# Kernel tuning notes

Measured on AMD Instinct MI355X. Metric: run time of the kernel, lower is better.

Reference implementation:

```python
import jax, jax.numpy as jnp
import numpy as np

B, USER_DIM, ITEM_DIM, LATENT = 8192, 3706, 6040, 512


def setup_inputs() -> dict:
    key = jax.random.key(0)
    kx, kwu, kwi = jax.random.split(key, 3)
    scale_u = 1.0 / np.sqrt(USER_DIM)
    scale_i = 1.0 / np.sqrt(ITEM_DIM)
    return {
        "x": jax.random.normal(kx, (B, USER_DIM + ITEM_DIM), dtype=jnp.float32),
        "Wu": jax.random.normal(kwu, (LATENT, USER_DIM), dtype=jnp.float32) * scale_u,
        "bu": jnp.zeros((LATENT,), dtype=jnp.float32),
        "Wi": jax.random.normal(kwi, (LATENT, ITEM_DIM), dtype=jnp.float32) * scale_i,
        "bi": jnp.zeros((LATENT,), dtype=jnp.float32),
    }


def reference(x, Wu, bu, Wi, bi):
    # mDA encode: linear + relu for each tower
    user_emb = jax.nn.relu(x[:, :USER_DIM] @ Wu.T + bu)   # [B, LATENT]
    item_emb = jax.nn.relu(x[:, -ITEM_DIM:] @ Wi.T + bi)  # [B, LATENT]
    # torch.mm(u, i.T).diag() == row-wise dot product (same math, O(B*d) not O(B^2*d))
    diag = jnp.einsum("bd,bd->b", user_emb, item_emb)     # [B]
    return diag[:, None]                                   # [B, 1]
```

## Files before the change

kernel.cpp:

```cpp
#include <hip/hip_runtime.h>
#include <hip/hip_bf16.h>
#include <stdint.h>

#define USER_DIM 3706
#define ITEM_DIM 6040
#define LATENT   512
#define BATCH    8192
#define XCOLS    (USER_DIM + ITEM_DIM)
#define KPAD_U   3712
#define KPAD_I   6144

typedef float f32x4 __attribute__((ext_vector_type(4)));
typedef short bf16x8 __attribute__((ext_vector_type(8)));

#define VMCNT(n) asm volatile("s_waitcnt vmcnt(" #n ")" ::: "memory")
#define LGKM0    asm volatile("s_waitcnt lgkmcnt(0)" ::: "memory")

static __device__ __forceinline__ unsigned short f2bf(float f) {
    union { float f; unsigned int u; } v; v.f = f;
    unsigned int u = v.u;
    u += 0x7fffu + ((u >> 16) & 1u);
    return (unsigned short)(u >> 16);
}
static __device__ __forceinline__ float bf2f(unsigned int b) {
    union { unsigned int u; float f; } v; v.u = b << 16; return v.f;
}
static __device__ __forceinline__ void gload16(const void* g, void* l) {
    __builtin_amdgcn_global_load_lds(
        (const __attribute__((address_space(1))) void*)g,
        (__attribute__((address_space(3))) void*)l, 16, 0, 0);
}
static __device__ __forceinline__ void BARRIER() {
    __builtin_amdgcn_sched_barrier(0);
    __builtin_amdgcn_s_barrier();
    __builtin_amdgcn_sched_barrier(0);
}

__global__ void convert_w(const float* __restrict__ W, unsigned short* __restrict__ Wb,
                          int K, int Kpad) {
    int c = blockIdx.x * blockDim.x + threadIdx.x;
    int r = blockIdx.y;
    if (c >= Kpad) return;
    unsigned short o = 0;
    if (c < K) o = f2bf(W[(size_t)r * K + c]);
    Wb[(size_t)r * Kpad + c] = o;
}

__global__ __launch_bounds__(256, 3) void gemm_fused(
    const float* __restrict__ X,
    const unsigned short* __restrict__ WuB, const float* __restrict__ bu,
    const unsigned short* __restrict__ WiB,
    unsigned short* __restrict__ Uemb,
    unsigned short* __restrict__ P0, unsigned short* __restrict__ P1)
{
    __shared__ unsigned short sA2[2][64 * 64];
    __shared__ unsigned short sB2[2][64 * 64];

    const int tid  = threadIdx.x;
    const int lane = tid & 63;
    const int wid  = tid >> 6;
    const int wm   = wid >> 1;
    const int wn   = wid & 1;

    const int bid = blockIdx.x;
    const int swz = (bid & 7) * 96 + (bid >> 3);
    const int g4  = swz >> 2;
    const int nb  = swz & 3;

    int mb, k0, nt, xoff, Kpad;
    const unsigned short* WB;
    bool isUser; int kh = 0;
    if (g4 % 3 == 0) {
        isUser = true;  mb = g4 / 3;
        k0 = 0; nt = KPAD_U / 32; xoff = 0; Kpad = KPAD_U; WB = WuB;
    } else {
        const int q = g4 - (g4 / 3 + 1);
        isUser = false; mb = q >> 1; kh = q & 1;
        k0 = kh * 96; nt = 96; xoff = USER_DIM; Kpad = KPAD_I; WB = WiB;
    }

    const int l8  = lane >> 3;
    const int c8w = lane & 7;
    const int s8  = c8w ^ l8;
    const int spr = s8 >> 2;
    const int skc = (s8 & 3) * 8;

    float4 raf[2][2];

    auto ALOAD = [&](int t) {
        const int kb = t * 32;
        #pragma unroll
        for (int o = 0; o < 2; ++o) {
            const int sego = wid * 16 + o * 8 + l8;
            const int grow = mb * 128 + sego * 2 + spr;
            const int xc   = xoff + kb + skc;
            const float* s = X + (size_t)grow * XCOLS + xc;
            if (xc + 8 > XCOLS) s = X;
            raf[o][0] = *(const float4*)s;
            raf[o][1] = *(const float4*)(s + 4);
        }
    };
    auto AWRITE = [&](int buf) {
        unsigned short* sA = sA2[buf];
        #pragma unroll
        for (int o = 0; o < 2; ++o) {
            const int sego = wid * 16 + o * 8 + l8;
            uint4 w;
            w.x = (unsigned)f2bf(raf[o][0].x) | ((unsigned)f2bf(raf[o][0].y) << 16);
            w.y = (unsigned)f2bf(raf[o][0].z) | ((unsigned)f2bf(raf[o][0].w) << 16);
            w.z = (unsigned)f2bf(raf[o][1].x) | ((unsigned)f2bf(raf[o][1].y) << 16);
            w.w = (unsigned)f2bf(raf[o][1].z) | ((unsigned)f2bf(raf[o][1].w) << 16);
            *(uint4*)(sA + sego * 64 + c8w * 8) = w;
        }
    };
    auto ISSUE_B = [&](int t, int buf) {
        const int kb = t * 32;
        unsigned short* sB = sB2[buf];
        #pragma unroll
        for (int j = 0; j < 2; ++j) {
            const int i  = wid * 2 + j;
            const int rt = (i * 8 + l8) * 2 + spr;
            const unsigned short* s =
                WB + (size_t)(nb * 128 + rt) * Kpad + kb + skc;
            gload16(s, sB + i * 512);
        }
    };

    const int fr   = lane & 15;
    const int g    = lane >> 4;
    const int rc8  = ((((fr & 1) * 4) + g) ^ (fr >> 1)) * 8;
    const int aro  = (wm * 32 + (fr >> 1)) * 64 + rc8;
    const int bro  = (wn * 32 + (fr >> 1)) * 64 + rc8;

    f32x4 acc[4][4];
    #pragma unroll
    for (int i = 0; i < 4; ++i)
        #pragma unroll
        for (int j = 0; j < 4; ++j) acc[i][j] = (f32x4)0.0f;

    auto COMPUTE = [&](int buf) {
        const unsigned short* sA = sA2[buf];
        const unsigned short* sB = sB2[buf];
        bf16x8 af[4], bfr[4];
        #pragma unroll
        for (int mi = 0; mi < 4; ++mi)
            af[mi] = *(const bf16x8*)(sA + aro + mi * 512);
        #pragma unroll
        for (int ni = 0; ni < 4; ++ni)
            bfr[ni] = *(const bf16x8*)(sB + bro + ni * 512);
        __builtin_amdgcn_s_setprio(1);
        #pragma unroll
        for (int mi = 0; mi < 4; ++mi)
            #pragma unroll
            for (int ni = 0; ni < 4; ++ni)
                acc[mi][ni] = __builtin_amdgcn_mfma_f32_16x16x32_bf16(
                    af[mi], bfr[ni], acc[mi][ni], 0, 0, 0);
        __builtin_amdgcn_s_setprio(0);
    };

    ALOAD(k0);
    ISSUE_B(k0, 0);
    AWRITE(0);
    ALOAD(k0 + 1);
    LGKM0;
    VMCNT(4);
    BARRIER();
    ISSUE_B(k0 + 1, 1);

    #pragma unroll 2
    for (int t = 0; t < nt - 2; ++t) {
        const int cur = t & 1;
        COMPUTE(cur);
        AWRITE(cur ^ 1);
        ALOAD(k0 + t + 2);
        LGKM0;
        BARRIER();
        ISSUE_B(k0 + t + 2, cur);
        VMCNT(6);
        BARRIER();
    }
    COMPUTE(0);
    AWRITE(1);
    LGKM0;
    BARRIER();
    VMCNT(0);
    BARRIER();
    COMPUTE(1);

    const int cb = nb * 128 + wn * 64;
    const int rb = mb * 128 + wm * 64 + (lane >> 4) * 4;
    if (isUser) {
        #pragma unroll
        for (int ni = 0; ni < 4; ++ni) {
            const int col = cb + ni * 16 + fr;
            const float bv = bu[col];
            #pragma unroll
            for (int mi = 0; mi < 4; ++mi) {
                f32x4 v = acc[mi][ni];
                #pragma unroll
                for (int r = 0; r < 4; ++r) {
                    const int row = rb + mi * 16 + r;
                    Uemb[(size_t)row * LATENT + col] = f2bf(fmaxf(v[r] + bv, 0.0f));
                }
            }
        }
    } else {
        unsigned short* P = kh ? P1 : P0;
        #pragma unroll
        for (int ni = 0; ni < 4; ++ni) {
            const int col = cb + ni * 16 + fr;
            #pragma unroll
            for (int mi = 0; mi < 4; ++mi) {
                f32x4 v = acc[mi][ni];
                #pragma unroll
                for (int r = 0; r < 4; ++r) {
                    const int row = rb + mi * 16 + r;
                    P[(size_t)row * LATENT + col] = f2bf(v[r]);
                }
            }
        }
    }
}

__global__ void rowdot(const unsigned short* __restrict__ U,
                       const unsigned short* __restrict__ P0,
                       const unsigned short* __restrict__ P1,
                       const float* __restrict__ bi,
                       float* __restrict__ out) {
    const int lane = threadIdx.x & 63;
    const int w    = threadIdx.x >> 6;
    const int row  = blockIdx.x * 4 + w;
    const size_t base = (size_t)row * LATENT + lane * 8;
    const uint4 uv = *(const uint4*)(U  + base);
    const uint4 p0 = *(const uint4*)(P0 + base);
    const uint4 p1 = *(const uint4*)(P1 + base);
    const float4 b0 = *(const float4*)(bi + lane * 8);
    const float4 b1 = *(const float4*)(bi + lane * 8 + 4);
    const float bb[8] = {b0.x, b0.y, b0.z, b0.w, b1.x, b1.y, b1.z, b1.w};
    const unsigned int* up = (const unsigned int*)&uv;
    const unsigned int* q0 = (const unsigned int*)&p0;
    const unsigned int* q1 = (const unsigned int*)&p1;
    float acc = 0.0f;
    #pragma unroll
    for (int q = 0; q < 4; ++q) {
        float ilo = fmaxf(bf2f(q0[q] & 0xffffu) + bf2f(q1[q] & 0xffffu) + bb[2 * q], 0.0f);
        float ihi = fmaxf(bf2f(q0[q] >> 16)     + bf2f(q1[q] >> 16)     + bb[2 * q + 1], 0.0f);
        acc += bf2f(up[q] & 0xffffu) * ilo;
        acc += bf2f(up[q] >> 16)     * ihi;
    }
    #pragma unroll
    for (int off = 32; off >= 1; off >>= 1)
        acc += __shfl_xor(acc, off, 64);
    if (lane == 0) out[row] = acc;
}

extern "C" void kernel_launch(void* const* d_in, const int* in_sizes, int n_in,
                              void* d_out, int out_size, void* d_ws, size_t ws_size,
                              hipStream_t stream) {
    const float* x  = (const float*)d_in[0];
    const float* Wu = (const float*)d_in[1];
    const float* bu = (const float*)d_in[2];
    const float* Wi = (const float*)d_in[3];
    const float* bi = (const float*)d_in[4];
    float* out = (float*)d_out;

    unsigned short* WuB  = (unsigned short*)d_ws;
    unsigned short* WiB  = WuB + (size_t)LATENT * KPAD_U;
    unsigned short* Uemb = WiB + (size_t)LATENT * KPAD_I;
    unsigned short* P0   = Uemb + (size_t)BATCH * LATENT;
    unsigned short* P1   = P0   + (size_t)BATCH * LATENT;

    convert_w<<<dim3((KPAD_U + 255) / 256, LATENT), 256, 0, stream>>>(Wu, WuB, USER_DIM, KPAD_U);
    convert_w<<<dim3((KPAD_I + 255) / 256, LATENT), 256, 0, stream>>>(Wi, WiB, ITEM_DIM, KPAD_I);

    gemm_fused<<<768, 256, 0, stream>>>(x, WuB, bu, WiB, Uemb, P0, P1);

    rowdot<<<BATCH / 4, 256, 0, stream>>>(Uemb, P0, P1, bi, out);
}
```

Baseline: 222.6 us.

## Load A fragments directly into registers, quad-buffer B in LDS

The A operand (fp32 X) no longer passes through LDS. Each lane loads its MFMA fragment straight from global memory and converts it to bf16 in registers, which removes the LDS writes and reads for A along with one barrier per iteration. B gets a four-slot LDS ring so only one barrier per k-step is needed, and the item-tower padded K shrinks from 6144 to 6080 to cut wasted tiles. The risk is less coalesced global loads for A, since each lane reads 32 contiguous bytes per row across 16 rows, plus more register pressure and a possible LDS reuse race given the relaxed synchronisation.

```diff
diff --git a/kernel.cpp b/kernel.cpp
--- a/kernel.cpp
+++ b/kernel.cpp
@@ -8,13 +8,12 @@
 #define BATCH    8192
 #define XCOLS    (USER_DIM + ITEM_DIM)
 #define KPAD_U   3712
-#define KPAD_I   6144
+#define KPAD_I   6080
 
 typedef float f32x4 __attribute__((ext_vector_type(4)));
 typedef short bf16x8 __attribute__((ext_vector_type(8)));
 
 #define VMCNT(n) asm volatile("s_waitcnt vmcnt(" #n ")" ::: "memory")
-#define LGKM0    asm volatile("s_waitcnt lgkmcnt(0)" ::: "memory")
 
 static __device__ __forceinline__ unsigned short f2bf(float f) {
     union { float f; unsigned int u; } v; v.f = f;
@@ -24,6 +23,17 @@
 }
 static __device__ __forceinline__ float bf2f(unsigned int b) {
     union { unsigned int u; float f; } v; v.u = b << 16; return v.f;
+}
+static __device__ __forceinline__ short cvt1(float f) {
+    union { __hip_bfloat16 h; unsigned short u; } cv;
+    cv.h = __float2bfloat16(f);
+    return (short)cv.u;
+}
+static __device__ __forceinline__ bf16x8 cvt8(f32x4 lo, f32x4 hi) {
+    bf16x8 r;
+    #pragma unroll
+    for (int i = 0; i < 4; ++i) { r[i] = cvt1(lo[i]); r[4 + i] = cvt1(hi[i]); }
+    return r;
 }
 static __device__ __forceinline__ void gload16(const void* g, void* l) {
     __builtin_amdgcn_global_load_lds(
@@ -53,8 +63,7 @@
     unsigned short* __restrict__ Uemb,
     unsigned short* __restrict__ P0, unsigned short* __restrict__ P1)
 {
-    __shared__ unsigned short sA2[2][64 * 64];
-    __shared__ unsigned short sB2[2][64 * 64];
+    __shared__ unsigned short sB4[4][64 * 64];
 
     const int tid  = threadIdx.x;
     const int lane = tid & 63;
@@ -76,7 +85,7 @@
     } else {
         const int q = g4 - (g4 / 3 + 1);
         isUser = false; mb = q >> 1; kh = q & 1;
-        k0 = kh * 96; nt = 96; xoff = USER_DIM; Kpad = KPAD_I; WB = WiB;
+        k0 = kh * 95; nt = 95; xoff = USER_DIM; Kpad = KPAD_I; WB = WiB;
     }
 
     const int l8  = lane >> 3;
@@ -85,37 +94,9 @@
     const int spr = s8 >> 2;
     const int skc = (s8 & 3) * 8;
 
-    float4 raf[2][2];
-
-    auto ALOAD = [&](int t) {
-        const int kb = t * 32;
-        #pragma unroll
-        for (int o = 0; o < 2; ++o) {
-            const int sego = wid * 16 + o * 8 + l8;
-            const int grow = mb * 128 + sego * 2 + spr;
-            const int xc   = xoff + kb + skc;
-            const float* s = X + (size_t)grow * XCOLS + xc;
-            if (xc + 8 > XCOLS) s = X;
-            raf[o][0] = *(const float4*)s;
-            raf[o][1] = *(const float4*)(s + 4);
-        }
-    };
-    auto AWRITE = [&](int buf) {
-        unsigned short* sA = sA2[buf];
-        #pragma unroll
-        for (int o = 0; o < 2; ++o) {
-            const int sego = wid * 16 + o * 8 + l8;
-            uint4 w;
-            w.x = (unsigned)f2bf(raf[o][0].x) | ((unsigned)f2bf(raf[o][0].y) << 16);
-            w.y = (unsigned)f2bf(raf[o][0].z) | ((unsigned)f2bf(raf[o][0].w) << 16);
-            w.z = (unsigned)f2bf(raf[o][1].x) | ((unsigned)f2bf(raf[o][1].y) << 16);
-            w.w = (unsigned)f2bf(raf[o][1].z) | ((unsigned)f2bf(raf[o][1].w) << 16);
-            *(uint4*)(sA + sego * 64 + c8w * 8) = w;
-        }
-    };
     auto ISSUE_B = [&](int t, int buf) {
         const int kb = t * 32;
-        unsigned short* sB = sB2[buf];
+        unsigned short* sB = sB4[buf];
         #pragma unroll
         for (int j = 0; j < 2; ++j) {
             const int i  = wid * 2 + j;
@@ -126,11 +107,31 @@
         }
     };
 
-    const int fr   = lane & 15;
-    const int g    = lane >> 4;
-    const int rc8  = ((((fr & 1) * 4) + g) ^ (fr >> 1)) * 8;
-    const int aro  = (wm * 32 + (fr >> 1)) * 64 + rc8;
-    const int bro  = (wn * 32 + (fr >> 1)) * 64 + rc8;
+    const int fr = lane & 15;
+    const int g  = lane >> 4;
+    const float* pA0 = X + (size_t)(mb * 128 + wm * 64 + 0  * 16 + fr) * XCOLS;
+    const float* pA1 = X + (size_t)(mb * 128 + wm * 64 + 1  * 16 + fr) * XCOLS;
+    const float* pA2 = X + (size_t)(mb * 128 + wm * 64 + 2  * 16 + fr) * XCOLS;
+    const float* pA3 = X + (size_t)(mb * 128 + wm * 64 + 3  * 16 + fr) * XCOLS;
+
+    f32x4 rafl[4], rafh[4];
+    bf16x8 af[4];
+
+    auto ALOAD = [&](int t) {
+        int kidx = xoff + t * 32 + g * 8;
+        if (kidx > XCOLS - 8) kidx = XCOLS - 8;
+        rafl[0] = *(const f32x4*)(pA0 + kidx); rafh[0] = *(const f32x4*)(pA0 + kidx + 4);
+        rafl[1] = *(const f32x4*)(pA1 + kidx); rafh[1] = *(const f32x4*)(pA1 + kidx + 4);
+        rafl[2] = *(const f32x4*)(pA2 + kidx); rafh[2] = *(const f32x4*)(pA2 + kidx + 4);
+        rafl[3] = *(const f32x4*)(pA3 + kidx); rafh[3] = *(const f32x4*)(pA3 + kidx + 4);
+    };
+    auto ACVT = [&]() {
+        #pragma unroll
+        for (int mi = 0; mi < 4; ++mi) af[mi] = cvt8(rafl[mi], rafh[mi]);
+    };
+
+    const int rc8 = ((((fr & 1) * 4) + g) ^ (fr >> 1)) * 8;
+    const int bro = (wn * 32 + (fr >> 1)) * 64 + rc8;
 
     f32x4 acc[4][4];
     #pragma unroll
@@ -139,12 +140,8 @@
         for (int j = 0; j < 4; ++j) acc[i][j] = (f32x4)0.0f;
 
     auto COMPUTE = [&](int buf) {
-        const unsigned short* sA = sA2[buf];
-        const unsigned short* sB = sB2[buf];
-        bf16x8 af[4], bfr[4];
-        #pragma unroll
-        for (int mi = 0; mi < 4; ++mi)
-            af[mi] = *(const bf16x8*)(sA + aro + mi * 512);
+        const unsigned short* sB = sB4[buf];
+        bf16x8 bfr[4];
         #pragma unroll
         for (int ni = 0; ni < 4; ++ni)
             bfr[ni] = *(const bf16x8*)(sB + bro + ni * 512);
@@ -160,32 +157,25 @@
 
     ALOAD(k0);
     ISSUE_B(k0, 0);
-    AWRITE(0);
+    ACVT();
     ALOAD(k0 + 1);
-    LGKM0;
-    VMCNT(4);
+    ISSUE_B(k0 + 1, 1);
+    VMCNT(10);
     BARRIER();
-    ISSUE_B(k0 + 1, 1);
-
-    #pragma unroll 2
+
     for (int t = 0; t < nt - 2; ++t) {
-        const int cur = t & 1;
-        COMPUTE(cur);
-        AWRITE(cur ^ 1);
+        COMPUTE(t & 3);
+        ACVT();
         ALOAD(k0 + t + 2);
-        LGKM0;
+        ISSUE_B(k0 + t + 2, (t + 2) & 3);
+        VMCNT(10);
         BARRIER();
-        ISSUE_B(k0 + t + 2, cur);
-        VMCNT(6);
-        BARRIER();
-    }
-    COMPUTE(0);
-    AWRITE(1);
-    LGKM0;
-    BARRIER();
+    }
+    COMPUTE((nt - 2) & 3);
+    ACVT();
     VMCNT(0);
     BARRIER();
-    COMPUTE(1);
+    COMPUTE((nt - 1) & 3);
 
     const int cb = nb * 128 + wn * 64;
     const int rb = mb * 128 + wm * 64 + (lane >> 4) * 4;
```

Result: slower. 324.2 us (+45.6%).

## Deepen GEMM prefetch pipeline to three stages with four B slots

Applied to the files above, without the earlier changes.

Restructures the main K loop so activation loads run three tiles ahead in register sets and weight tiles run three ahead in a four-slot LDS ring. The loop is unrolled by three with a drain epilogue, and KPAD_U is padded so the user tower's tile count fits the unroll. The aim is to hide more global-memory latency on the fp32 X stream and the bf16 weight stream. In exchange it uses more registers and LDS, which could lower occupancy under launch_bounds(256,3), and the padded user K adds zero-tile work.

```diff
diff --git a/kernel.cpp b/kernel.cpp
--- a/kernel.cpp
+++ b/kernel.cpp
@@ -7,7 +7,7 @@
 #define LATENT   512
 #define BATCH    8192
 #define XCOLS    (USER_DIM + ITEM_DIM)
-#define KPAD_U   3712
+#define KPAD_U   3744
 #define KPAD_I   6144
 
 typedef float f32x4 __attribute__((ext_vector_type(4)));
@@ -54,7 +54,7 @@
     unsigned short* __restrict__ P0, unsigned short* __restrict__ P1)
 {
     __shared__ unsigned short sA2[2][64 * 64];
-    __shared__ unsigned short sB2[2][64 * 64];
+    __shared__ unsigned short sB4[4][64 * 64];
 
     const int tid  = threadIdx.x;
     const int lane = tid & 63;
@@ -67,16 +67,16 @@
     const int g4  = swz >> 2;
     const int nb  = swz & 3;
 
-    int mb, k0, nt, xoff, Kpad;
+    int mb, k0s, nt, xoff, Kpad;
     const unsigned short* WB;
     bool isUser; int kh = 0;
     if (g4 % 3 == 0) {
         isUser = true;  mb = g4 / 3;
-        k0 = 0; nt = KPAD_U / 32; xoff = 0; Kpad = KPAD_U; WB = WuB;
+        k0s = 0; nt = KPAD_U / 32; xoff = 0; Kpad = KPAD_U; WB = WuB;
     } else {
         const int q = g4 - (g4 / 3 + 1);
         isUser = false; mb = q >> 1; kh = q & 1;
-        k0 = kh * 96; nt = 96; xoff = USER_DIM; Kpad = KPAD_I; WB = WiB;
+        k0s = kh * 96; nt = 96; xoff = USER_DIM; Kpad = KPAD_I; WB = WiB;
     }
 
     const int l8  = lane >> 3;
@@ -85,37 +85,35 @@
     const int spr = s8 >> 2;
     const int skc = (s8 & 3) * 8;
 
-    float4 raf[2][2];
-
-    auto ALOAD = [&](int t) {
-        const int kb = t * 32;
-        #pragma unroll
-        for (int o = 0; o < 2; ++o) {
-            const int sego = wid * 16 + o * 8 + l8;
-            const int grow = mb * 128 + sego * 2 + spr;
-            const int xc   = xoff + kb + skc;
-            const float* s = X + (size_t)grow * XCOLS + xc;
-            if (xc + 8 > XCOLS) s = X;
-            raf[o][0] = *(const float4*)s;
-            raf[o][1] = *(const float4*)(s + 4);
-        }
-    };
-    auto AWRITE = [&](int buf) {
+    const int asg0 = wid * 16 + l8;
+    const float* aptr0 = X + (size_t)(mb * 128 + asg0 * 2 + spr) * XCOLS + xoff;
+    const float* aptr1 = aptr0 + (size_t)16 * XCOLS;
+
+    auto ALOAD = [&](f32x4 (&R)[4], int tk) {
+        int kc = tk * 32 + skc;
+        if (xoff + kc + 8 > XCOLS) kc = XCOLS - xoff - 8;
+        R[0] = *(const f32x4*)(aptr0 + kc);
+        R[1] = *(const f32x4*)(aptr0 + kc + 4);
+        R[2] = *(const f32x4*)(aptr1 + kc);
+        R[3] = *(const f32x4*)(aptr1 + kc + 4);
+    };
+    auto AWRITE = [&](const f32x4 (&R)[4], int buf) {
         unsigned short* sA = sA2[buf];
-        #pragma unroll
-        for (int o = 0; o < 2; ++o) {
-            const int sego = wid * 16 + o * 8 + l8;
-            uint4 w;
-            w.x = (unsigned)f2bf(raf[o][0].x) | ((unsigned)f2bf(raf[o][0].y) << 16);
-            w.y = (unsigned)f2bf(raf[o][0].z) | ((unsigned)f2bf(raf[o][0].w) << 16);
-            w.z = (unsigned)f2bf(raf[o][1].x) | ((unsigned)f2bf(raf[o][1].y) << 16);
-            w.w = (unsigned)f2bf(raf[o][1].z) | ((unsigned)f2bf(raf[o][1].w) << 16);
-            *(uint4*)(sA + sego * 64 + c8w * 8) = w;
-        }
-    };
-    auto ISSUE_B = [&](int t, int buf) {
-        const int kb = t * 32;
-        unsigned short* sB = sB2[buf];
+        uint4 w0, w1;
+        w0.x = (unsigned)f2bf(R[0].x) | ((unsigned)f2bf(R[0].y) << 16);
+        w0.y = (unsigned)f2bf(R[0].z) | ((unsigned)f2bf(R[0].w) << 16);
+        w0.z = (unsigned)f2bf(R[1].x) | ((unsigned)f2bf(R[1].y) << 16);
+        w0.w = (unsigned)f2bf(R[1].z) | ((unsigned)f2bf(R[1].w) << 16);
+        w1.x = (unsigned)f2bf(R[2].x) | ((unsigned)f2bf(R[2].y) << 16);
+        w1.y = (unsigned)f2bf(R[2].z) | ((unsigned)f2bf(R[2].w) << 16);
+        w1.z = (unsigned)f2bf(R[3].x) | ((unsigned)f2bf(R[3].y) << 16);
+        w1.w = (unsigned)f2bf(R[3].z) | ((unsigned)f2bf(R[3].w) << 16);
+        *(uint4*)(sA + asg0 * 64 + c8w * 8) = w0;
+        *(uint4*)(sA + (asg0 + 8) * 64 + c8w * 8) = w1;
+    };
+    auto ISSUE_B = [&](int tk, int slot) {
+        const int kb = tk * 32;
+        unsigned short* sB = sB4[slot];
         #pragma unroll
         for (int j = 0; j < 2; ++j) {
             const int i  = wid * 2 + j;
@@ -126,11 +124,11 @@
         }
     };
 
-    const int fr   = lane & 15;
-    const int g    = lane >> 4;
-    const int rc8  = ((((fr & 1) * 4) + g) ^ (fr >> 1)) * 8;
-    const int aro  = (wm * 32 + (fr >> 1)) * 64 + rc8;
-    const int bro  = (wn * 32 + (fr >> 1)) * 64 + rc8;
+    const int fr  = lane & 15;
+    const int g   = lane >> 4;
+    const int lro = (fr >> 1) * 64 + ((((fr & 1) * 4) + g) ^ (fr >> 1)) * 8;
+    const int aro = wm * 2048 + lro;
+    const int bro = wn * 2048 + lro;
 
     f32x4 acc[4][4];
     #pragma unroll
@@ -138,9 +136,9 @@
         #pragma unroll
         for (int j = 0; j < 4; ++j) acc[i][j] = (f32x4)0.0f;
 
-    auto COMPUTE = [&](int buf) {
-        const unsigned short* sA = sA2[buf];
-        const unsigned short* sB = sB2[buf];
+    auto COMPUTE = [&](int abuf, int slot) {
+        const unsigned short* sA = sA2[abuf];
+        const unsigned short* sB = sB4[slot];
         bf16x8 af[4], bfr[4];
         #pragma unroll
         for (int mi = 0; mi < 4; ++mi)
@@ -158,34 +156,56 @@
         __builtin_amdgcn_s_setprio(0);
     };
 
-    ALOAD(k0);
-    ISSUE_B(k0, 0);
-    AWRITE(0);
-    ALOAD(k0 + 1);
+    f32x4 rs0[4], rs1[4], rs2[4];
+
+    ALOAD(rs0, k0s + 0); ISSUE_B(k0s + 0, 0);
+    ALOAD(rs1, k0s + 1); ISSUE_B(k0s + 1, 1);
+    ALOAD(rs2, k0s + 2); ISSUE_B(k0s + 2, 2);
+    AWRITE(rs0, 0);
     LGKM0;
-    VMCNT(4);
+    VMCNT(12);
     BARRIER();
-    ISSUE_B(k0 + 1, 1);
-
-    #pragma unroll 2
-    for (int t = 0; t < nt - 2; ++t) {
-        const int cur = t & 1;
-        COMPUTE(cur);
-        AWRITE(cur ^ 1);
-        ALOAD(k0 + t + 2);
+
+    #define GSTEP(T, SW, SL)                                   \
+    {                                                          \
+        const int t_ = (T);                                    \
+        COMPUTE(t_ & 1, t_ & 3);                               \
+        AWRITE(SW, (t_ + 1) & 1);      \
+        ALOAD(SL, k0s + t_ + 3);                               \
+        LGKM0;                                                 \
+        BARRIER();                                             \
+        ISSUE_B(k0s + t_ + 3, (t_ + 3) & 3);                   \
+        VMCNT(12);                                             \
+        BARRIER();                                             \
+    }
+
+    for (int T = 0; T + 5 < nt; T += 3) {
+        GSTEP(T,     rs1, rs0)
+        GSTEP(T + 1, rs2, rs1)
+        GSTEP(T + 2, rs0, rs2)
+    }
+    #undef GSTEP
+
+    {
+        const int t0 = nt - 3;
+        COMPUTE(t0 & 1, t0 & 3);
+        AWRITE(rs1, (t0 + 1) & 1);
         LGKM0;
         BARRIER();
-        ISSUE_B(k0 + t + 2, cur);
         VMCNT(6);
         BARRIER();
-    }
-    COMPUTE(0);
-    AWRITE(1);
-    LGKM0;
-    BARRIER();
-    VMCNT(0);
-    BARRIER();
-    COMPUTE(1);
+
+        const int t1 = nt - 2;
+        COMPUTE(t1 & 1, t1 & 3);
+        AWRITE(rs2, (t1 + 1) & 1);
+        LGKM0;
+        BARRIER();
+        VMCNT(0);
+        BARRIER();
+
+        const int t2 = nt - 1;
+        COMPUTE(t2 & 1, t2 & 3);
+    }
 
     const int cb = nb * 128 + wn * 64;
     const int rb = mb * 128 + wm * 64 + (lane >> 4) * 4;
```

Result: slower. 281.3 us (+26.4%).
